# Kernel optimization log

Hardware: AMD Instinct MI355X
Metric: run time of the kernel (lower is better)

Reference implementation:

```python
import jax, jax.numpy as jnp
import numpy as np

N = 20000      # nodes
E = 320000     # edges (before self-loops)
C_IN, C_HID, C_OUT = 256, 256, 128
NEG_SLOPE = 0.2  # PyG GATConv default


def setup_inputs() -> dict:
    key = jax.random.key(0)
    ks = jax.random.split(key, 10)
    x = jax.random.normal(ks[0], (N, C_IN), dtype=jnp.float32)
    edge_index = jax.random.randint(ks[1], (2, E), 0, N, dtype=jnp.int64)

    def glorot(k, shape, fan):
        return jax.random.normal(k, shape, dtype=jnp.float32) / np.float32(np.sqrt(fan))

    W1 = glorot(ks[2], (C_IN, C_HID), C_IN)
    a_src1 = glorot(ks[3], (C_HID,), C_HID)
    a_dst1 = glorot(ks[4], (C_HID,), C_HID)
    b1 = jnp.zeros((C_HID,), jnp.float32)
    W2 = glorot(ks[5], (C_HID, C_OUT), C_HID)
    a_src2 = glorot(ks[6], (C_OUT,), C_OUT)
    a_dst2 = glorot(ks[7], (C_OUT,), C_OUT)
    b2 = jnp.zeros((C_OUT,), jnp.float32)
    return dict(x=x, edge_index=edge_index, W1=W1, a_src1=a_src1, a_dst1=a_dst1,
                b1=b1, W2=W2, a_src2=a_src2, a_dst2=a_dst2, b2=b2)


def gat_layer(x, src, dst, W, a_src, a_dst, b, n):
    # PyG GATConv (heads=1): linear proj, additive attention, softmax over
    # incoming edges per destination node, weighted aggregation + bias.
    h = x @ W                                   # [N, F]
    alpha_src = h @ a_src                       # [N]
    alpha_dst = h @ a_dst                       # [N]
    e = jax.nn.leaky_relu(alpha_src[src] + alpha_dst[dst], NEG_SLOPE)  # [E]
    m = jax.ops.segment_max(e, dst, num_segments=n)                    # stable softmax
    e = jnp.exp(e - m[dst])
    denom = jax.ops.segment_sum(e, dst, num_segments=n)                # [N]
    out = jax.ops.segment_sum(e[:, None] * h[src], dst, num_segments=n)  # [N, F]
    return out / denom[:, None] + b


def reference(x, edge_index, W1, a_src1, a_dst1, b1, W2, a_src2, a_dst2, b2):
    n = x.shape[0]
    # GATConv adds self-loops by default
    loops = jnp.arange(n, dtype=edge_index.dtype)
    ei = jnp.concatenate([edge_index, jnp.stack([loops, loops])], axis=1)
    src, dst = ei[0], ei[1]
    h = gat_layer(x, src, dst, W1, a_src1, a_dst1, b1, n)
    h = jax.nn.relu(h)  # Dropout is identity in eval mode
    return gat_layer(h, src, dst, W2, a_src2, a_dst2, b2, n)
```

## Files before the change

### kernel.cpp

```cpp
#include <hip/hip_runtime.h>
#include <math.h>

#define N_NODES 20000
#define N_EDGES 320000
#define C_IN  256
#define C_HID 256
#define C_OUT 128
#define NEG_SLOPE 0.2f
#define CAP   256
#define GEMM1_BLKS (N_NODES / 32)
#define SCAT_BLKS  ((N_EDGES + 255) / 256)

typedef __attribute__((ext_vector_type(8))) short bf16x8;
typedef __attribute__((ext_vector_type(4))) float f32x4;

__device__ __align__(16) unsigned short c_W1h[C_IN * C_HID], c_W1l[C_IN * C_HID];
__device__ __align__(16) unsigned short c_W2h[C_HID * C_OUT], c_W2l[C_HID * C_OUT];
__device__ float c_as1f[C_HID], c_ad1f[C_HID], c_b1f[C_HID];
__device__ float c_as2f[C_OUT], c_ad2f[C_OUT], c_b2f[C_OUT];
__device__ __align__(16) unsigned short g_h1b[(size_t)N_NODES * C_HID];
__device__ __align__(16) unsigned short g_g1h[(size_t)N_NODES * C_HID];
__device__ __align__(16) unsigned short g_g1l[(size_t)N_NODES * C_HID];
__device__ __align__(16) unsigned short g_h2b[(size_t)N_NODES * C_OUT];
__device__ float g_alps1[N_NODES], g_alpd1[N_NODES];
__device__ float g_alps2[N_NODES], g_alpd2[N_NODES];
__device__ int   g_cursor[N_NODES];
__device__ int   g_srcidx[(size_t)N_NODES * CAP];
__device__ int   g_is64;
__device__ int   g_isf32;

__device__ __forceinline__ float bf2f(unsigned short b){
  unsigned int u = ((unsigned int)b) << 16;
  return __builtin_bit_cast(float, u);
}
__device__ __forceinline__ unsigned short f2bf(float f){
  unsigned int u = __builtin_bit_cast(unsigned int, f);
  u += 0x7fffu + ((u >> 16) & 1u);
  return (unsigned short)(u >> 16);
}
__device__ __forceinline__ int clampi(int v){
  v = v < 0 ? 0 : v;
  return v >= N_NODES ? N_NODES - 1 : v;
}
__device__ __forceinline__ void edge_sd(const int* ei, int e, int& s, int& d){
  if (g_is64){ s = ei[2 * e]; d = ei[2 * (N_EDGES + e)]; }
  else       { s = ei[e];     d = ei[N_EDGES + e]; }
  s = clampi(s); d = clampi(d);
}

struct Ptrs { const void* p[8]; };

__device__ __forceinline__ int wpack(int k, int n, int Nc){
  return (((k >> 5) * (Nc / 16) + (n >> 4)) * 64 + (((k >> 3) & 3) * 16 + (n & 15))) * 8 + (k & 7);
}

#define PREP_Z  N_NODES
#define PREP_W1 (C_IN * C_HID)
#define PREP_W2 (C_HID * C_OUT)
#define PREP_T  (PREP_Z + PREP_W1 + PREP_W2 + 2 * C_HID + C_HID + 2 * C_OUT + C_OUT)

__global__ void prep_k(const unsigned int* __restrict__ xw,
                       const int* __restrict__ ei, Ptrs ps){
  __shared__ int s_isf32;
  if (threadIdx.x < 64){
    int lane = (int)threadIdx.x, cnt = 0;
    for (int j = lane; j < 256; j += 64){
      unsigned int e = (xw[j] >> 7) & 0xFFu;
      if (e >= 0x60u && e <= 0x8Fu) ++cnt;
    }
#pragma unroll
    for (int o = 32; o > 0; o >>= 1) cnt += __shfl_xor(cnt, o, 64);
    if (lane == 0) s_isf32 = (cnt < 200) ? 1 : 0;
  }
  __syncthreads();
  const int isf32 = s_isf32;

  if (blockIdx.x == 0 && threadIdx.x < 64){
    unsigned long long anybad = __ballot(ei[2 * (int)threadIdx.x + 1] != 0);
    if (threadIdx.x == 0){ g_isf32 = isf32; g_is64 = (anybad == 0ULL) ? 1 : 0; }
  }

  int tid = (int)(blockIdx.x * blockDim.x + threadIdx.x);
  if (tid < PREP_Z){
    g_cursor[tid] = 0;
    g_alps1[tid] = 0.f; g_alpd1[tid] = 0.f;
    g_alps2[tid] = 0.f; g_alpd2[tid] = 0.f;
    return;
  }
  int j = tid - PREP_Z;
  auto ld = [&](const void* p, int i) -> float {
    return isf32 ? ((const float*)p)[i] : bf2f(((const unsigned short*)p)[i]);
  };
  if (j < PREP_W1){
    float f = ld(ps.p[0], j);
    int k = j / C_HID, n = j % C_HID;
    int idx = wpack(k, n, C_HID);
    unsigned short h = f2bf(f);
    c_W1h[idx] = h; c_W1l[idx] = f2bf(f - bf2f(h));
    return;
  }
  j -= PREP_W1;
  if (j < PREP_W2){
    float f = ld(ps.p[4], j);
    int k = j / C_OUT, n = j % C_OUT;
    int idx = wpack(k, n, C_OUT);
    unsigned short h = f2bf(f);
    c_W2h[idx] = h; c_W2l[idx] = f2bf(f - bf2f(h));
    return;
  }
  j -= PREP_W2;
  if      (j <  256) c_as1f[j]        = ld(ps.p[1], j);
  else if (j <  512) c_ad1f[j - 256]  = ld(ps.p[2], j - 256);
  else if (j <  768) c_b1f [j - 512]  = ld(ps.p[3], j - 512);
  else if (j <  896) c_as2f[j - 768]  = ld(ps.p[5], j - 768);
  else if (j < 1024) c_ad2f[j - 896]  = ld(ps.p[6], j - 896);
  else if (j < 1152) c_b2f [j - 1024] = ld(ps.p[7], j - 1024);
}

template<int SEL>
__global__ __launch_bounds__(256) void gemm_k(const void* __restrict__ xsrc,
                                              const int* __restrict__ ei){
  if (SEL == 0 && blockIdx.x >= GEMM1_BLKS){
    int e = (int)(blockIdx.x - GEMM1_BLKS) * 256 + (int)threadIdx.x;
    if (e < N_EDGES){
      int s, d;
      edge_sd(ei, e, s, d);
      int pos = atomicAdd(&g_cursor[d], 1);
      if (pos < CAP) g_srcidx[(size_t)d * CAP + pos] = s;
    }
    return;
  }

  const int Nc = SEL ? C_OUT : C_HID;
  const int NT = SEL ? 2 : 4;
  const unsigned short* Wh = SEL ? c_W2h : c_W1h;
  const unsigned short* Wl = SEL ? c_W2l : c_W1l;
  unsigned short* Hb = SEL ? g_h2b : g_h1b;
  float* alps = SEL ? g_alps2 : g_alps1;
  float* alpd = SEL ? g_alpd2 : g_alpd1;
  const float* aS = SEL ? c_as2f : c_as1f;
  const float* aD = SEL ? c_ad2f : c_ad1f;
  const bool isf32 = (SEL == 0) && (g_isf32 != 0);

  int wave = (int)(threadIdx.x >> 6);
  int lane = (int)(threadIdx.x & 63);
  int kgrp = lane >> 4, cl = lane & 15;
  int mbase = blockIdx.x * 32;

  f32x4 acc[2][4];
#pragma unroll
  for (int m = 0; m < 2; ++m)
#pragma unroll
    for (int n = 0; n < NT; ++n) acc[m][n] = (f32x4){0.f, 0.f, 0.f, 0.f};

  for (int kt = 0; kt < 8; ++kt){
    int kbase = kt * 32 + kgrp * 8;
    bf16x8 ah[2], al[2];
    if (SEL == 1){
#pragma unroll
      for (int m = 0; m < 2; ++m){
        size_t ai = (size_t)(mbase + m * 16 + cl) * 256 + kbase;
        ah[m] = *(const bf16x8*)(g_g1h + ai);
        al[m] = *(const bf16x8*)(g_g1l + ai);
      }
    } else if (isf32){
      const float* Xf = (const float*)xsrc;
#pragma unroll
      for (int m = 0; m < 2; ++m){
        const float4* xp = (const float4*)(Xf + (size_t)(mbase + m * 16 + cl) * 256 + kbase);
        float4 v0 = xp[0], v1 = xp[1];
        float vals[8] = {v0.x, v0.y, v0.z, v0.w, v1.x, v1.y, v1.z, v1.w};
#pragma unroll
        for (int j = 0; j < 8; ++j){
          unsigned short h = f2bf(vals[j]);
          ah[m][j] = (short)h;
          al[m][j] = (short)f2bf(vals[j] - bf2f(h));
        }
      }
    } else {
      const unsigned short* Xb = (const unsigned short*)xsrc;
#pragma unroll
      for (int m = 0; m < 2; ++m){
        ah[m] = *(const bf16x8*)(Xb + (size_t)(mbase + m * 16 + cl) * 256 + kbase);
        al[m] = (bf16x8){0,0,0,0,0,0,0,0};
      }
    }
#pragma unroll
    for (int nn = 0; nn < NT; ++nn){
      int nt = wave * NT + nn;
      size_t wi = ((size_t)(kt * (Nc / 16) + nt) * 64 + lane) * 8;
      bf16x8 bh = *(const bf16x8*)(Wh + wi);
      bf16x8 bl = *(const bf16x8*)(Wl + wi);
#pragma unroll
      for (int m = 0; m < 2; ++m){
        acc[m][nn] = __builtin_amdgcn_mfma_f32_16x16x32_bf16(ah[m], bh, acc[m][nn], 0, 0, 0);
        acc[m][nn] = __builtin_amdgcn_mfma_f32_16x16x32_bf16(ah[m], bl, acc[m][nn], 0, 0, 0);
        acc[m][nn] = __builtin_amdgcn_mfma_f32_16x16x32_bf16(al[m], bh, acc[m][nn], 0, 0, 0);
      }
    }
  }

  float asv[4], adv[4];
#pragma unroll
  for (int nn = 0; nn < NT; ++nn){
    int col = (wave * NT + nn) * 16 + cl;
    asv[nn] = aS[col]; adv[nn] = aD[col];
  }
#pragma unroll
  for (int m = 0; m < 2; ++m){
#pragma unroll
    for (int i = 0; i < 4; ++i){
      int row = mbase + m * 16 + kgrp * 4 + i;
      float ps = 0.f, pd = 0.f;
#pragma unroll
      for (int nn = 0; nn < NT; ++nn){
        int col = (wave * NT + nn) * 16 + cl;
        float v = acc[m][nn][i];
        Hb[(size_t)row * Nc + col] = f2bf(v);
        ps += v * asv[nn]; pd += v * adv[nn];
      }
      ps += __shfl_xor(ps, 1);  pd += __shfl_xor(pd, 1);
      ps += __shfl_xor(ps, 2);  pd += __shfl_xor(pd, 2);
      ps += __shfl_xor(ps, 4);  pd += __shfl_xor(pd, 4);
      ps += __shfl_xor(ps, 8);  pd += __shfl_xor(pd, 8);
      if (cl == 0){
        atomicAdd(&alps[row], ps);
        atomicAdd(&alpd[row], pd);
      }
    }
  }
}

#define ACC4(p, ww) { \
  a0 += (ww) * bf2f((unsigned short)((p).x & 0xFFFFu)); \
  a1 += (ww) * bf2f((unsigned short)((p).x >> 16)); \
  a2 += (ww) * bf2f((unsigned short)((p).y & 0xFFFFu)); \
  a3 += (ww) * bf2f((unsigned short)((p).y >> 16)); }

#define ACC2(p, ww) { \
  a0 += (ww) * bf2f((unsigned short)((p) & 0xFFFFu)); \
  a1 += (ww) * bf2f((unsigned short)((p) >> 16)); }

template<int F, int SEL>
__global__ void agg_k(float* OUT){
  const unsigned short* Hb = SEL ? g_h2b : g_h1b;
  const float* bias = SEL ? c_b2f : c_b1f;
  const float* alps = SEL ? g_alps2 : g_alps1;
  const float* alpd = SEL ? g_alpd2 : g_alpd1;
  int lane = threadIdx.x & 63;
  int n = blockIdx.x * 4 + (threadIdx.x >> 6);
  int len = g_cursor[n]; if (len > CAP) len = CAP;
  int i0 = n * CAP, i1 = i0 + len;
  float adn = alpd[n];
  float dpart = 0.f;
  float a0 = 0.f, a1 = 0.f, a2 = 0.f, a3 = 0.f;
  const uint2* H2 = (const uint2*)Hb;
  const unsigned int* H1 = (const unsigned int*)Hb;

  {
    float es = alps[n] + adn;
    es = (es > 0.f) ? es : NEG_SLOPE * es;
    float wself = __expf(es);
    if (lane == 0) dpart += wself;
    if constexpr (F == 256){
      uint2 p = H2[(size_t)n * 64 + lane];
      ACC4(p, wself)
    } else {
      unsigned int p = H1[(size_t)n * 64 + lane];
      ACC2(p, wself)
    }
  }

  for (int base = i0; base < i1; base += 64){
    int nv = i1 - base; if (nv > 64) nv = 64;
    int sv = 0; float wv = 0.f;
    if (lane < nv){
      sv = g_srcidx[base + lane];
      float e = alps[sv] + adn;
      e = (e > 0.f) ? e : NEG_SLOPE * e;
      wv = __expf(e);
    }
    dpart += wv;
    int j = 0;
    for (; j + 8 <= nv; j += 8){
      int s0 = __shfl(sv, j),     s1 = __shfl(sv, j + 1);
      int s2 = __shfl(sv, j + 2), s3 = __shfl(sv, j + 3);
      int s4 = __shfl(sv, j + 4), s5 = __shfl(sv, j + 5);
      int s6 = __shfl(sv, j + 6), s7 = __shfl(sv, j + 7);
      float w0 = __shfl(wv, j),     w1 = __shfl(wv, j + 1);
      float w2 = __shfl(wv, j + 2), w3 = __shfl(wv, j + 3);
      float w4 = __shfl(wv, j + 4), w5 = __shfl(wv, j + 5);
      float w6 = __shfl(wv, j + 6), w7 = __shfl(wv, j + 7);
      if constexpr (F == 256){
        uint2 p0 = H2[(size_t)s0 * 64 + lane];
        uint2 p1 = H2[(size_t)s1 * 64 + lane];
        uint2 p2 = H2[(size_t)s2 * 64 + lane];
        uint2 p3 = H2[(size_t)s3 * 64 + lane];
        uint2 p4 = H2[(size_t)s4 * 64 + lane];
        uint2 p5 = H2[(size_t)s5 * 64 + lane];
        uint2 p6 = H2[(size_t)s6 * 64 + lane];
        uint2 p7 = H2[(size_t)s7 * 64 + lane];
        ACC4(p0, w0) ACC4(p1, w1) ACC4(p2, w2) ACC4(p3, w3)
        ACC4(p4, w4) ACC4(p5, w5) ACC4(p6, w6) ACC4(p7, w7)
      } else {
        unsigned int p0 = H1[(size_t)s0 * 64 + lane];
        unsigned int p1 = H1[(size_t)s1 * 64 + lane];
        unsigned int p2 = H1[(size_t)s2 * 64 + lane];
        unsigned int p3 = H1[(size_t)s3 * 64 + lane];
        unsigned int p4 = H1[(size_t)s4 * 64 + lane];
        unsigned int p5 = H1[(size_t)s5 * 64 + lane];
        unsigned int p6 = H1[(size_t)s6 * 64 + lane];
        unsigned int p7 = H1[(size_t)s7 * 64 + lane];
        ACC2(p0, w0) ACC2(p1, w1) ACC2(p2, w2) ACC2(p3, w3)
        ACC2(p4, w4) ACC2(p5, w5) ACC2(p6, w6) ACC2(p7, w7)
      }
    }
    for (; j + 4 <= nv; j += 4){
      int s0 = __shfl(sv, j),     s1 = __shfl(sv, j + 1);
      int s2 = __shfl(sv, j + 2), s3 = __shfl(sv, j + 3);
      float w0 = __shfl(wv, j),     w1 = __shfl(wv, j + 1);
      float w2 = __shfl(wv, j + 2), w3 = __shfl(wv, j + 3);
      if constexpr (F == 256){
        uint2 p0 = H2[(size_t)s0 * 64 + lane];
        uint2 p1 = H2[(size_t)s1 * 64 + lane];
        uint2 p2 = H2[(size_t)s2 * 64 + lane];
        uint2 p3 = H2[(size_t)s3 * 64 + lane];
        ACC4(p0, w0) ACC4(p1, w1) ACC4(p2, w2) ACC4(p3, w3)
      } else {
        unsigned int p0 = H1[(size_t)s0 * 64 + lane];
        unsigned int p1 = H1[(size_t)s1 * 64 + lane];
        unsigned int p2 = H1[(size_t)s2 * 64 + lane];
        unsigned int p3 = H1[(size_t)s3 * 64 + lane];
        ACC2(p0, w0) ACC2(p1, w1) ACC2(p2, w2) ACC2(p3, w3)
      }
    }
    for (; j < nv; ++j){
      int s = __shfl(sv, j);
      float w = __shfl(wv, j);
      if constexpr (F == 256){
        uint2 p = H2[(size_t)s * 64 + lane];
        ACC4(p, w)
      } else {
        unsigned int p = H1[(size_t)s * 64 + lane];
        ACC2(p, w)
      }
    }
  }

  float den = dpart;
#pragma unroll
  for (int o = 32; o > 0; o >>= 1) den += __shfl_xor(den, o, 64);
  float inv = 1.f / den;

  if constexpr (F == 256){
    float o0 = a0 * inv + bias[4 * lane];
    float o1 = a1 * inv + bias[4 * lane + 1];
    float o2 = a2 * inv + bias[4 * lane + 2];
    float o3 = a3 * inv + bias[4 * lane + 3];
    if (SEL == 0){
      o0 = fmaxf(o0, 0.f); o1 = fmaxf(o1, 0.f);
      o2 = fmaxf(o2, 0.f); o3 = fmaxf(o3, 0.f);
      unsigned short h0 = f2bf(o0), h1 = f2bf(o1), h2 = f2bf(o2), h3 = f2bf(o3);
      uint2 ph, pl;
      ph.x = (unsigned)h0 | ((unsigned)h1 << 16);
      ph.y = (unsigned)h2 | ((unsigned)h3 << 16);
      pl.x = (unsigned)f2bf(o0 - bf2f(h0)) | ((unsigned)f2bf(o1 - bf2f(h1)) << 16);
      pl.y = (unsigned)f2bf(o2 - bf2f(h2)) | ((unsigned)f2bf(o3 - bf2f(h3)) << 16);
      ((uint2*)g_g1h)[(size_t)n * 64 + lane] = ph;
      ((uint2*)g_g1l)[(size_t)n * 64 + lane] = pl;
    } else {
      float4 o; o.x = o0; o.y = o1; o.z = o2; o.w = o3;
      ((float4*)OUT)[(size_t)n * 64 + lane] = o;
    }
  } else {
    float o0 = a0 * inv + bias[2 * lane];
    float o1 = a1 * inv + bias[2 * lane + 1];
    if (SEL == 0){
      o0 = fmaxf(o0, 0.f); o1 = fmaxf(o1, 0.f);
      unsigned short h0 = f2bf(o0), h1 = f2bf(o1);
      ((unsigned int*)g_g1h)[(size_t)n * 64 + lane] = (unsigned)h0 | ((unsigned)h1 << 16);
      ((unsigned int*)g_g1l)[(size_t)n * 64 + lane] =
        (unsigned)f2bf(o0 - bf2f(h0)) | ((unsigned)f2bf(o1 - bf2f(h1)) << 16);
    } else {
      float2 o; o.x = o0; o.y = o1;
      ((float2*)OUT)[(size_t)n * 64 + lane] = o;
    }
  }
}

extern "C" void kernel_launch(void* const* d_in, const int* in_sizes, int n_in,
                              void* d_out, int out_size, void* d_ws, size_t ws_size,
                              hipStream_t stream){
  (void)in_sizes; (void)n_in; (void)out_size; (void)d_ws; (void)ws_size;
  const void* x  = d_in[0];
  const int*  ei = (const int*)d_in[1];
  float* out = (float*)d_out;

  Ptrs ps;
  ps.p[0] = d_in[2]; ps.p[1] = d_in[3]; ps.p[2] = d_in[4]; ps.p[3] = d_in[5];
  ps.p[4] = d_in[6]; ps.p[5] = d_in[7]; ps.p[6] = d_in[8]; ps.p[7] = d_in[9];

  prep_k<<<(PREP_T + 255) / 256, 256, 0, stream>>>((const unsigned int*)x, ei, ps);

  gemm_k<0><<<GEMM1_BLKS + SCAT_BLKS, 256, 0, stream>>>(x, ei);
  agg_k<C_HID, 0><<<N_NODES / 4, 256, 0, stream>>>(nullptr);

  gemm_k<1><<<N_NODES / 32, 256, 0, stream>>>(nullptr, nullptr);
  agg_k<C_OUT, 1><<<N_NODES / 4, 256, 0, stream>>>(out);
}
```

Measured before the change: 180.7 us.

## Fuse layer-1 aggregation with layer-2 GEMM through shared memory

Merges the first-layer aggregation kernel and the second-layer projection GEMM into one kernel. Each block aggregates 16 nodes, stores the split hi/lo bf16 hidden rows in padded LDS, then runs the MFMA GEMM and attention dot products straight from LDS. This removes the global round trip of the two N x 256 bf16 buffers, one launch, and the atomics on alps2/alpd2. The cost is that each wave handles four nodes serially, so fewer blocks run with more LDS per block, which could lower latency hiding in the gather phase.

```diff
diff --git a/kernel.cpp b/kernel.cpp
--- a/kernel.cpp
+++ b/kernel.cpp
@@ -10,6 +10,7 @@
 #define CAP   256
 #define GEMM1_BLKS (N_NODES / 32)
 #define SCAT_BLKS  ((N_EDGES + 255) / 256)
+#define AGG_PAD 280
 
 typedef __attribute__((ext_vector_type(8))) short bf16x8;
 typedef __attribute__((ext_vector_type(4))) float f32x4;
@@ -19,8 +20,6 @@
 __device__ float c_as1f[C_HID], c_ad1f[C_HID], c_b1f[C_HID];
 __device__ float c_as2f[C_OUT], c_ad2f[C_OUT], c_b2f[C_OUT];
 __device__ __align__(16) unsigned short g_h1b[(size_t)N_NODES * C_HID];
-__device__ __align__(16) unsigned short g_g1h[(size_t)N_NODES * C_HID];
-__device__ __align__(16) unsigned short g_g1l[(size_t)N_NODES * C_HID];
 __device__ __align__(16) unsigned short g_h2b[(size_t)N_NODES * C_OUT];
 __device__ float g_alps1[N_NODES], g_alpd1[N_NODES];
 __device__ float g_alps2[N_NODES], g_alpd2[N_NODES];
@@ -117,10 +116,9 @@
   else if (j < 1152) c_b2f [j - 1024] = ld(ps.p[7], j - 1024);
 }
 
-template<int SEL>
-__global__ __launch_bounds__(256) void gemm_k(const void* __restrict__ xsrc,
-                                              const int* __restrict__ ei){
-  if (SEL == 0 && blockIdx.x >= GEMM1_BLKS){
+__global__ __launch_bounds__(256) void gemm1_k(const void* __restrict__ xsrc,
+                                               const int* __restrict__ ei){
+  if (blockIdx.x >= GEMM1_BLKS){
     int e = (int)(blockIdx.x - GEMM1_BLKS) * 256 + (int)threadIdx.x;
     if (e < N_EDGES){
       int s, d;
@@ -131,18 +129,8 @@
     return;
   }
 
-  const int Nc = SEL ? C_OUT : C_HID;
-  const int NT = SEL ? 2 : 4;
-  const unsigned short* Wh = SEL ? c_W2h : c_W1h;
-  const unsigned short* Wl = SEL ? c_W2l : c_W1l;
-  unsigned short* Hb = SEL ? g_h2b : g_h1b;
-  float* alps = SEL ? g_alps2 : g_alps1;
-  float* alpd = SEL ? g_alpd2 : g_alpd1;
-  const float* aS = SEL ? c_as2f : c_as1f;
-  const float* aD = SEL ? c_ad2f : c_ad1f;
-  const bool isf32 = (SEL == 0) && (g_isf32 != 0);
-
-  int wave = (int)(threadIdx.x >> 6);
+  const bool isf32 = (g_isf32 != 0);
+  int wid  = (int)(threadIdx.x >> 6);
   int lane = (int)(threadIdx.x & 63);
   int kgrp = lane >> 4, cl = lane & 15;
   int mbase = blockIdx.x * 32;
@@ -151,19 +139,12 @@
 #pragma unroll
   for (int m = 0; m < 2; ++m)
 #pragma unroll
-    for (int n = 0; n < NT; ++n) acc[m][n] = (f32x4){0.f, 0.f, 0.f, 0.f};
+    for (int n = 0; n < 4; ++n) acc[m][n] = (f32x4){0.f, 0.f, 0.f, 0.f};
 
   for (int kt = 0; kt < 8; ++kt){
     int kbase = kt * 32 + kgrp * 8;
     bf16x8 ah[2], al[2];
-    if (SEL == 1){
-#pragma unroll
-      for (int m = 0; m < 2; ++m){
-        size_t ai = (size_t)(mbase + m * 16 + cl) * 256 + kbase;
-        ah[m] = *(const bf16x8*)(g_g1h + ai);
-        al[m] = *(const bf16x8*)(g_g1l + ai);
-      }
-    } else if (isf32){
+    if (isf32){
       const float* Xf = (const float*)xsrc;
 #pragma unroll
       for (int m = 0; m < 2; ++m){
@@ -186,11 +167,11 @@
       }
     }
 #pragma unroll
-    for (int nn = 0; nn < NT; ++nn){
-      int nt = wave * NT + nn;
-      size_t wi = ((size_t)(kt * (Nc / 16) + nt) * 64 + lane) * 8;
-      bf16x8 bh = *(const bf16x8*)(Wh + wi);
-      bf16x8 bl = *(const bf16x8*)(Wl + wi);
+    for (int nn = 0; nn < 4; ++nn){
+      int nt = wid * 4 + nn;
+      size_t wi = ((size_t)(kt * 16 + nt) * 64 + lane) * 8;
+      bf16x8 bh = *(const bf16x8*)(c_W1h + wi);
+      bf16x8 bl = *(const bf16x8*)(c_W1l + wi);
 #pragma unroll
       for (int m = 0; m < 2; ++m){
         acc[m][nn] = __builtin_amdgcn_mfma_f32_16x16x32_bf16(ah[m], bh, acc[m][nn], 0, 0, 0);
@@ -202,9 +183,9 @@
 
   float asv[4], adv[4];
 #pragma unroll
-  for (int nn = 0; nn < NT; ++nn){
-    int col = (wave * NT + nn) * 16 + cl;
-    asv[nn] = aS[col]; adv[nn] = aD[col];
+  for (int nn = 0; nn < 4; ++nn){
+    int col = (wid * 4 + nn) * 16 + cl;
+    asv[nn] = c_as1f[col]; adv[nn] = c_ad1f[col];
   }
 #pragma unroll
   for (int m = 0; m < 2; ++m){
@@ -213,10 +194,10 @@
       int row = mbase + m * 16 + kgrp * 4 + i;
       float ps = 0.f, pd = 0.f;
 #pragma unroll
-      for (int nn = 0; nn < NT; ++nn){
-        int col = (wave * NT + nn) * 16 + cl;
+      for (int nn = 0; nn < 4; ++nn){
+        int col = (wid * 4 + nn) * 16 + cl;
         float v = acc[m][nn][i];
-        Hb[(size_t)row * Nc + col] = f2bf(v);
+        g_h1b[(size_t)row * C_HID + col] = f2bf(v);
         ps += v * asv[nn]; pd += v * adv[nn];
       }
       ps += __shfl_xor(ps, 1);  pd += __shfl_xor(pd, 1);
@@ -224,8 +205,8 @@
       ps += __shfl_xor(ps, 4);  pd += __shfl_xor(pd, 4);
       ps += __shfl_xor(ps, 8);  pd += __shfl_xor(pd, 8);
       if (cl == 0){
-        atomicAdd(&alps[row], ps);
-        atomicAdd(&alpd[row], pd);
+        atomicAdd(&g_alps1[row], ps);
+        atomicAdd(&g_alpd1[row], pd);
       }
     }
   }
@@ -241,34 +222,174 @@
   a0 += (ww) * bf2f((unsigned short)((p) & 0xFFFFu)); \
   a1 += (ww) * bf2f((unsigned short)((p) >> 16)); }
 
-template<int F, int SEL>
-__global__ void agg_k(float* OUT){
-  const unsigned short* Hb = SEL ? g_h2b : g_h1b;
-  const float* bias = SEL ? c_b2f : c_b1f;
-  const float* alps = SEL ? g_alps2 : g_alps1;
-  const float* alpd = SEL ? g_alpd2 : g_alpd1;
-  int lane = threadIdx.x & 63;
-  int n = blockIdx.x * 4 + (threadIdx.x >> 6);
+__global__ __launch_bounds__(256) void aggemm_k(){
+  __shared__ __align__(16) unsigned short s_hi[16 * AGG_PAD];
+  __shared__ __align__(16) unsigned short s_lo[16 * AGG_PAD];
+  __shared__ float s_ps[4][16], s_pd[4][16];
+
+  int lane = (int)(threadIdx.x & 63);
+  int wid  = (int)(threadIdx.x >> 6);
+  int nb   = blockIdx.x * 16;
+  const uint2* H2 = (const uint2*)g_h1b;
+
+  for (int q = 0; q < 4; ++q){
+    int n = nb + wid * 4 + q;
+    int len = g_cursor[n]; if (len > CAP) len = CAP;
+    int i0 = n * CAP, i1 = i0 + len;
+    float adn = g_alpd1[n];
+    float dpart = 0.f;
+    float a0 = 0.f, a1 = 0.f, a2 = 0.f, a3 = 0.f;
+
+    {
+      float es = g_alps1[n] + adn;
+      es = (es > 0.f) ? es : NEG_SLOPE * es;
+      float wself = __expf(es);
+      if (lane == 0) dpart += wself;
+      uint2 p = H2[(size_t)n * 64 + lane];
+      ACC4(p, wself)
+    }
+
+    for (int base = i0; base < i1; base += 64){
+      int nv = i1 - base; if (nv > 64) nv = 64;
+      int sv = 0; float wv = 0.f;
+      if (lane < nv){
+        sv = g_srcidx[base + lane];
+        float e = g_alps1[sv] + adn;
+        e = (e > 0.f) ? e : NEG_SLOPE * e;
+        wv = __expf(e);
+      }
+      dpart += wv;
+      int j = 0;
+      for (; j + 8 <= nv; j += 8){
+        int s0 = __shfl(sv, j),     s1 = __shfl(sv, j + 1);
+        int s2 = __shfl(sv, j + 2), s3 = __shfl(sv, j + 3);
+        int s4 = __shfl(sv, j + 4), s5 = __shfl(sv, j + 5);
+        int s6 = __shfl(sv, j + 6), s7 = __shfl(sv, j + 7);
+        float w0 = __shfl(wv, j),     w1 = __shfl(wv, j + 1);
+        float w2 = __shfl(wv, j + 2), w3 = __shfl(wv, j + 3);
+        float w4 = __shfl(wv, j + 4), w5 = __shfl(wv, j + 5);
+        float w6 = __shfl(wv, j + 6), w7 = __shfl(wv, j + 7);
+        uint2 p0 = H2[(size_t)s0 * 64 + lane];
+        uint2 p1 = H2[(size_t)s1 * 64 + lane];
+        uint2 p2 = H2[(size_t)s2 * 64 + lane];
+        uint2 p3 = H2[(size_t)s3 * 64 + lane];
+        uint2 p4 = H2[(size_t)s4 * 64 + lane];
+        uint2 p5 = H2[(size_t)s5 * 64 + lane];
+        uint2 p6 = H2[(size_t)s6 * 64 + lane];
+        uint2 p7 = H2[(size_t)s7 * 64 + lane];
+        ACC4(p0, w0) ACC4(p1, w1) ACC4(p2, w2) ACC4(p3, w3)
+        ACC4(p4, w4) ACC4(p5, w5) ACC4(p6, w6) ACC4(p7, w7)
+      }
+      for (; j + 4 <= nv; j += 4){
+        int s0 = __shfl(sv, j),     s1 = __shfl(sv, j + 1);
+        int s2 = __shfl(sv, j + 2), s3 = __shfl(sv, j + 3);
+        float w0 = __shfl(wv, j),     w1 = __shfl(wv, j + 1);
+        float w2 = __shfl(wv, j + 2), w3 = __shfl(wv, j + 3);
+        uint2 p0 = H2[(size_t)s0 * 64 + lane];
+        uint2 p1 = H2[(size_t)s1 * 64 + lane];
+        uint2 p2 = H2[(size_t)s2 * 64 + lane];
+        uint2 p3 = H2[(size_t)s3 * 64 + lane];
+        ACC4(p0, w0) ACC4(p1, w1) ACC4(p2, w2) ACC4(p3, w3)
+      }
+      for (; j < nv; ++j){
+        int s = __shfl(sv, j);
+        float w = __shfl(wv, j);
+        uint2 p = H2[(size_t)s * 64 + lane];
+        ACC4(p, w)
+      }
+    }
+
+    float den = dpart;
+#pragma unroll
+    for (int o = 32; o > 0; o >>= 1) den += __shfl_xor(den, o, 64);
+    float inv = 1.f / den;
+
+    float o0 = a0 * inv + c_b1f[4 * lane];
+    float o1 = a1 * inv + c_b1f[4 * lane + 1];
+    float o2 = a2 * inv + c_b1f[4 * lane + 2];
+    float o3 = a3 * inv + c_b1f[4 * lane + 3];
+    o0 = fmaxf(o0, 0.f); o1 = fmaxf(o1, 0.f);
+    o2 = fmaxf(o2, 0.f); o3 = fmaxf(o3, 0.f);
+    unsigned short h0 = f2bf(o0), h1 = f2bf(o1), h2 = f2bf(o2), h3 = f2bf(o3);
+    uint2 ph, pl;
+    ph.x = (unsigned)h0 | ((unsigned)h1 << 16);
+    ph.y = (unsigned)h2 | ((unsigned)h3 << 16);
+    pl.x = (unsigned)f2bf(o0 - bf2f(h0)) | ((unsigned)f2bf(o1 - bf2f(h1)) << 16);
+    pl.y = (unsigned)f2bf(o2 - bf2f(h2)) | ((unsigned)f2bf(o3 - bf2f(h3)) << 16);
+    int r = wid * 4 + q;
+    *(uint2*)&s_hi[r * AGG_PAD + 4 * lane] = ph;
+    *(uint2*)&s_lo[r * AGG_PAD + 4 * lane] = pl;
+  }
+  __syncthreads();
+
+  int kgrp = lane >> 4, cl = lane & 15;
+  f32x4 acc[2];
+  acc[0] = (f32x4){0.f, 0.f, 0.f, 0.f};
+  acc[1] = (f32x4){0.f, 0.f, 0.f, 0.f};
+  for (int kt = 0; kt < 8; ++kt){
+    int rb = cl * AGG_PAD + kt * 32 + kgrp * 8;
+    bf16x8 ah = *(const bf16x8*)&s_hi[rb];
+    bf16x8 al = *(const bf16x8*)&s_lo[rb];
+#pragma unroll
+    for (int nn = 0; nn < 2; ++nn){
+      int nt = wid * 2 + nn;
+      size_t wi = ((size_t)(kt * 8 + nt) * 64 + lane) * 8;
+      bf16x8 bh = *(const bf16x8*)(c_W2h + wi);
+      bf16x8 bl = *(const bf16x8*)(c_W2l + wi);
+      acc[nn] = __builtin_amdgcn_mfma_f32_16x16x32_bf16(ah, bh, acc[nn], 0, 0, 0);
+      acc[nn] = __builtin_amdgcn_mfma_f32_16x16x32_bf16(ah, bl, acc[nn], 0, 0, 0);
+      acc[nn] = __builtin_amdgcn_mfma_f32_16x16x32_bf16(al, bh, acc[nn], 0, 0, 0);
+    }
+  }
+
+  float asv[2], adv[2];
+#pragma unroll
+  for (int nn = 0; nn < 2; ++nn){
+    int col = (wid * 2 + nn) * 16 + cl;
+    asv[nn] = c_as2f[col]; adv[nn] = c_ad2f[col];
+  }
+#pragma unroll
+  for (int i = 0; i < 4; ++i){
+    int row = nb + kgrp * 4 + i;
+    float ps = 0.f, pd = 0.f;
+#pragma unroll
+    for (int nn = 0; nn < 2; ++nn){
+      int col = (wid * 2 + nn) * 16 + cl;
+      float v = acc[nn][i];
+      g_h2b[(size_t)row * C_OUT + col] = f2bf(v);
+      ps += v * asv[nn]; pd += v * adv[nn];
+    }
+    ps += __shfl_xor(ps, 1);  pd += __shfl_xor(pd, 1);
+    ps += __shfl_xor(ps, 2);  pd += __shfl_xor(pd, 2);
+    ps += __shfl_xor(ps, 4);  pd += __shfl_xor(pd, 4);
+    ps += __shfl_xor(ps, 8);  pd += __shfl_xor(pd, 8);
+    if (cl == 0){ s_ps[wid][kgrp * 4 + i] = ps; s_pd[wid][kgrp * 4 + i] = pd; }
+  }
+  __syncthreads();
+  if (threadIdx.x < 16){
+    int r = (int)threadIdx.x;
+    g_alps2[nb + r] = s_ps[0][r] + s_ps[1][r] + s_ps[2][r] + s_ps[3][r];
+    g_alpd2[nb + r] = s_pd[0][r] + s_pd[1][r] + s_pd[2][r] + s_pd[3][r];
+  }
+}
+
+__global__ void agg2_k(float* OUT){
+  int lane = (int)(threadIdx.x & 63);
+  int n = blockIdx.x * 4 + (int)(threadIdx.x >> 6);
   int len = g_cursor[n]; if (len > CAP) len = CAP;
   int i0 = n * CAP, i1 = i0 + len;
-  float adn = alpd[n];
+  float adn = g_alpd2[n];
   float dpart = 0.f;
-  float a0 = 0.f, a1 = 0.f, a2 = 0.f, a3 = 0.f;
-  const uint2* H2 = (const uint2*)Hb;
-  const unsigned int* H1 = (const unsigned int*)Hb;
+  float a0 = 0.f, a1 = 0.f;
+  const unsigned int* H1 = (const unsigned int*)g_h2b;
 
   {
-    float es = alps[n] + adn;
+    float es = g_alps2[n] + adn;
     es = (es > 0.f) ? es : NEG_SLOPE * es;
     float wself = __expf(es);
     if (lane == 0) dpart += wself;
-    if constexpr (F == 256){
-      uint2 p = H2[(size_t)n * 64 + lane];
-      ACC4(p, wself)
-    } else {
-      unsigned int p = H1[(size_t)n * 64 + lane];
-      ACC2(p, wself)
-    }
+    unsigned int p = H1[(size_t)n * 64 + lane];
+    ACC2(p, wself)
   }
 
   for (int base = i0; base < i1; base += 64){
@@ -276,7 +397,7 @@
     int sv = 0; float wv = 0.f;
     if (lane < nv){
       sv = g_srcidx[base + lane];
-      float e = alps[sv] + adn;
+      float e = g_alps2[sv] + adn;
       e = (e > 0.f) ? e : NEG_SLOPE * e;
       wv = __expf(e);
     }
@@ -291,59 +412,33 @@
       float w2 = __shfl(wv, j + 2), w3 = __shfl(wv, j + 3);
       float w4 = __shfl(wv, j + 4), w5 = __shfl(wv, j + 5);
       float w6 = __shfl(wv, j + 6), w7 = __shfl(wv, j + 7);
-      if constexpr (F == 256){
-        uint2 p0 = H2[(size_t)s0 * 64 + lane];
-        uint2 p1 = H2[(size_t)s1 * 64 + lane];
-        uint2 p2 = H2[(size_t)s2 * 64 + lane];
-        uint2 p3 = H2[(size_t)s3 * 64 + lane];
-        uint2 p4 = H2[(size_t)s4 * 64 + lane];
-        uint2 p5 = H2[(size_t)s5 * 64 + lane];
-        uint2 p6 = H2[(size_t)s6 * 64 + lane];
-        uint2 p7 = H2[(size_t)s7 * 64 + lane];
-        ACC4(p0, w0) ACC4(p1, w1) ACC4(p2, w2) ACC4(p3, w3)
-        ACC4(p4, w4) ACC4(p5, w5) ACC4(p6, w6) ACC4(p7, w7)
-      } else {
-        unsigned int p0 = H1[(size_t)s0 * 64 + lane];
-        unsigned int p1 = H1[(size_t)s1 * 64 + lane];
-        unsigned int p2 = H1[(size_t)s2 * 64 + lane];
-        unsigned int p3 = H1[(size_t)s3 * 64 + lane];
-        unsigned int p4 = H1[(size_t)s4 * 64 + lane];
-        unsigned int p5 = H1[(size_t)s5 * 64 + lane];
-        unsigned int p6 = H1[(size_t)s6 * 64 + lane];
-        unsigned int p7 = H1[(size_t)s7 * 64 + lane];
-        ACC2(p0, w0) ACC2(p1, w1) ACC2(p2, w2) ACC2(p3, w3)
-        ACC2(p4, w4) ACC2(p5, w5) ACC2(p6, w6) ACC2(p7, w7)
-      }
+      unsigned int p0 = H1[(size_t)s0 * 64 + lane];
+      unsigned int p1 = H1[(size_t)s1 * 64 + lane];
+      unsigned int p2 = H1[(size_t)s2 * 64 + lane];
+      unsigned int p3 = H1[(size_t)s3 * 64 + lane];
+      unsigned int p4 = H1[(size_t)s4 * 64 + lane];
+      unsigned int p5 = H1[(size_t)s5 * 64 + lane];
+      unsigned int p6 = H1[(size_t)s6 * 64 + lane];
+      unsigned int p7 = H1[(size_t)s7 * 64 + lane];
+      ACC2(p0, w0) ACC2(p1, w1) ACC2(p2, w2) ACC2(p3, w3)
+      ACC2(p4, w4) ACC2(p5, w5) ACC2(p6, w6) ACC2(p7, w7)
     }
     for (; j + 4 <= nv; j += 4){
       int s0 = __shfl(sv, j),     s1 = __shfl(sv, j + 1);
       int s2 = __shfl(sv, j + 2), s3 = __shfl(sv, j + 3);
       float w0 = __shfl(wv, j),     w1 = __shfl(wv, j + 1);
       float w2 = __shfl(wv, j + 2), w3 = __shfl(wv, j + 3);
-      if constexpr (F == 256){
-        uint2 p0 = H2[(size_t)s0 * 64 + lane];
-        uint2 p1 = H2[(size_t)s1 * 64 + lane];
-        uint2 p2 = H2[(size_t)s2 * 64 + lane];
-        uint2 p3 = H2[(size_t)s3 * 64 + lane];
-        ACC4(p0, w0) ACC4(p1, w1) ACC4(p2, w2) ACC4(p3, w3)
-      } else {
-        unsigned int p0 = H1[(size_t)s0 * 64 + lane];
-        unsigned int p1 = H1[(size_t)s1 * 64 + lane];
-        unsigned int p2 = H1[(size_t)s2 * 64 + lane];
-        unsigned int p3 = H1[(size_t)s3 * 64 + lane];
-        ACC2(p0, w0) ACC2(p1, w1) ACC2(p2, w2) ACC2(p3, w3)
-      }
+      unsigned int p0 = H1[(size_t)s0 * 64 + lane];
+      unsigned int p1 = H1[(size_t)s1 * 64 + lane];
+      unsigned int p2 = H1[(size_t)s2 * 64 + lane];
+      unsigned int p3 = H1[(size_t)s3 * 64 + lane];
+      ACC2(p0, w0) ACC2(p1, w1) ACC2(p2, w2) ACC2(p3, w3)
     }
     for (; j < nv; ++j){
       int s = __shfl(sv, j);
       float w = __shfl(wv, j);
-      if constexpr (F == 256){
-        uint2 p = H2[(size_t)s * 64 + lane];
-        ACC4(p, w)
-      } else {
-        unsigned int p = H1[(size_t)s * 64 + lane];
-        ACC2(p, w)
-      }
+      unsigned int p = H1[(size_t)s * 64 + lane];
+      ACC2(p, w)
     }
   }
 
@@ -352,40 +447,10 @@
   for (int o = 32; o > 0; o >>= 1) den += __shfl_xor(den, o, 64);
   float inv = 1.f / den;
 
-  if constexpr (F == 256){
-    float o0 = a0 * inv + bias[4 * lane];
-    float o1 = a1 * inv + bias[4 * lane + 1];
-    float o2 = a2 * inv + bias[4 * lane + 2];
-    float o3 = a3 * inv + bias[4 * lane + 3];
-    if (SEL == 0){
-      o0 = fmaxf(o0, 0.f); o1 = fmaxf(o1, 0.f);
-      o2 = fmaxf(o2, 0.f); o3 = fmaxf(o3, 0.f);
-      unsigned short h0 = f2bf(o0), h1 = f2bf(o1), h2 = f2bf(o2), h3 = f2bf(o3);
-      uint2 ph, pl;
-      ph.x = (unsigned)h0 | ((unsigned)h1 << 16);
-      ph.y = (unsigned)h2 | ((unsigned)h3 << 16);
-      pl.x = (unsigned)f2bf(o0 - bf2f(h0)) | ((unsigned)f2bf(o1 - bf2f(h1)) << 16);
-      pl.y = (unsigned)f2bf(o2 - bf2f(h2)) | ((unsigned)f2bf(o3 - bf2f(h3)) << 16);
-      ((uint2*)g_g1h)[(size_t)n * 64 + lane] = ph;
-      ((uint2*)g_g1l)[(size_t)n * 64 + lane] = pl;
-    } else {
-      float4 o; o.x = o0; o.y = o1; o.z = o2; o.w = o3;
-      ((float4*)OUT)[(size_t)n * 64 + lane] = o;
-    }
-  } else {
-    float o0 = a0 * inv + bias[2 * lane];
-    float o1 = a1 * inv + bias[2 * lane + 1];
-    if (SEL == 0){
-      o0 = fmaxf(o0, 0.f); o1 = fmaxf(o1, 0.f);
-      unsigned short h0 = f2bf(o0), h1 = f2bf(o1);
-      ((unsigned int*)g_g1h)[(size_t)n * 64 + lane] = (unsigned)h0 | ((unsigned)h1 << 16);
-      ((unsigned int*)g_g1l)[(size_t)n * 64 + lane] =
-        (unsigned)f2bf(o0 - bf2f(h0)) | ((unsigned)f2bf(o1 - bf2f(h1)) << 16);
-    } else {
-      float2 o; o.x = o0; o.y = o1;
-      ((float2*)OUT)[(size_t)n * 64 + lane] = o;
-    }
-  }
+  float2 o;
+  o.x = a0 * inv + c_b2f[2 * lane];
+  o.y = a1 * inv + c_b2f[2 * lane + 1];
+  ((float2*)OUT)[(size_t)n * 64 + lane] = o;
 }
 
 extern "C" void kernel_launch(void* const* d_in, const int* in_sizes, int n_in,
@@ -402,9 +467,9 @@
 
   prep_k<<<(PREP_T + 255) / 256, 256, 0, stream>>>((const unsigned int*)x, ei, ps);
 
-  gemm_k<0><<<GEMM1_BLKS + SCAT_BLKS, 256, 0, stream>>>(x, ei);
-  agg_k<C_HID, 0><<<N_NODES / 4, 256, 0, stream>>>(nullptr);
-
-  gemm_k<1><<<N_NODES / 32, 256, 0, stream>>>(nullptr, nullptr);
-  agg_k<C_OUT, 1><<<N_NODES / 4, 256, 0, stream>>>(out);
-}
+  gemm1_k<<<GEMM1_BLKS + SCAT_BLKS, 256, 0, stream>>>(x, ei);
+
+  aggemm_k<<<N_NODES / 16, 256, 0, stream>>>();
+
+  agg2_k<<<N_NODES / 4, 256, 0, stream>>>(out);
+}
```

Result: faster. 165.6 us (-8.3%).
